# Optimization experiments

Measured on AMD Instinct MI355X. Metric: run time of the kernel, lower is better.

## Reference

```python
import jax, jax.numpy as jnp
import numpy as np

N_DIMS = 256
HW = 32
FILTERS = [32, 64, 128, 256]
SCALES = [16, 8, 4, 2]
B = 4


def _ds(t, s):
    # Exact bilinear downsample (align_corners=False, half-pixel centers) by even integer factor s:
    # target coord (i+0.5)*s - 0.5 = s*i + s/2 - 0.5 -> mean of neighbours s*i+s//2-1 and s*i+s//2.
    if s == 1:
        return t
    oH, oW = t.shape[2] // s, t.shape[3] // s
    ih = jnp.arange(oH) * s + s // 2 - 1
    iw = jnp.arange(oW) * s + s // 2 - 1
    t = 0.5 * (t[:, :, ih, :] + t[:, :, ih + 1, :])
    t = 0.5 * (t[:, :, :, iw] + t[:, :, :, iw + 1])
    return t


def _spp(t, s, w, scale, bias):
    # Upsample(1/s) -> Conv3x3(no bias) -> BN(folded to scale/bias, eval form) -> ReLU
    t = _ds(t, s)
    t = jax.lax.conv_general_dilated(t, w, (1, 1), 'SAME',
                                     dimension_numbers=('NCHW', 'OIHW', 'NCHW'))
    return jax.nn.relu(t * scale[None, :, None, None] + bias[None, :, None, None])


def setup_inputs() -> dict:
    key = jax.random.key(0)
    ks = iter(jax.random.split(key, 32))
    d = {}
    d['x'] = jax.random.normal(next(ks), (B, N_DIMS, HW, HW), jnp.float32)
    sizes = [HW * s for s in SCALES]
    for i, (c, sz) in enumerate(zip(FILTERS, sizes)):
        d[f'x{i}'] = jax.random.normal(next(ks), (B, c, sz, sz), jnp.float32)
    for i, c in enumerate(FILTERS):
        d[f'w{i}'] = jax.random.normal(next(ks), (N_DIMS, c, 3, 3), jnp.float32) * (1.0 / np.sqrt(9 * c))
        d[f's{i}'] = jax.random.normal(next(ks), (N_DIMS,), jnp.float32) * 0.1 + 1.0
        d[f'b{i}'] = jax.random.normal(next(ks), (N_DIMS,), jnp.float32) * 0.1
    dq = N_DIMS // 8
    d['qw'] = jax.random.normal(next(ks), (dq, N_DIMS), jnp.float32) * (1.0 / np.sqrt(N_DIMS))
    d['qb'] = jnp.zeros((dq,), jnp.float32)
    d['kw'] = jax.random.normal(next(ks), (dq, N_DIMS), jnp.float32) * (1.0 / np.sqrt(N_DIMS))
    d['kb'] = jnp.zeros((dq,), jnp.float32)
    d['vw'] = jax.random.normal(next(ks), (N_DIMS, N_DIMS), jnp.float32) * (1.0 / np.sqrt(N_DIMS))
    d['vb'] = jnp.zeros((N_DIMS,), jnp.float32)
    d['rel_h'] = jax.random.normal(next(ks), (1, dq, HW, 1), jnp.float32)
    d['rel_w'] = jax.random.normal(next(ks), (1, dq, 1, HW), jnp.float32)
    d['gamma'] = jax.random.normal(next(ks), (1,), jnp.float32) * 0.5  # torch inits to 0; nonzero for useful test
    return d


def reference(x, x0, x1, x2, x3,
              w0, s0, b0, w1, s1, b1, w2, s2, b2, w3, s3, b3,
              qw, qb, kw, kb, vw, vb, rel_h, rel_w, gamma):
    Bm, C, H, W = x.shape
    N = H * W
    multi_x = (_spp(x0, 16, w0, s0, b0) + _spp(x1, 8, w1, s1, b1)
               + _spp(x2, 4, w2, s2, b2) + _spp(x3, 2, w3, s3, b3))
    # 1x1 convs as channel matmuls
    q = jnp.einsum('bchw,oc->bohw', multi_x, qw) + qb[None, :, None, None]
    k = jnp.einsum('bchw,oc->bohw', x, kw) + kb[None, :, None, None]
    v = jnp.einsum('bchw,oc->bohw', x, vw) + vb[None, :, None, None]
    q = q.reshape(Bm, -1, N).transpose(0, 2, 1)          # [B, N, C/8]
    k = k.reshape(Bm, -1, N)                             # [B, C/8, N]
    v = v.reshape(Bm, C, N)                              # [B, C, N]
    energy = jnp.einsum('bnc,bcm->bnm', q, k)            # content
    pos = (rel_h + rel_w).reshape(C // 8, N)             # [C/8, N]
    energy = energy + jnp.einsum('bnc,cm->bnm', q, pos)  # + position bias
    attn = jax.nn.softmax(energy, axis=-1)               # [B, N, N]
    out = jnp.einsum('bcj,bij->bci', v, attn).reshape(Bm, C, H, W)
    out = gamma * out + x
    return out, attn
```

## Files before the change

### kernel.cpp

```cpp
#include <hip/hip_runtime.h>
#include <stdint.h>

#define BN 4
#define CC 256
#define DQ 32
#define HWD 32
#define NN 1024

typedef __attribute__((ext_vector_type(8))) short short8v;
typedef __attribute__((ext_vector_type(16))) float float16v;

#define W3OFF0 0
#define W3OFF1 73728
#define W3OFF2 221184
#define W3OFF3 516096
#define WQOFF  1105920
#define WKOFF  1114112
#define WVOFF  1122304
#define WPKTOT 1187840

#define PREP_PAD 8880
#define PREP_RPK 4640
#define PREP_XT  512
#define PREP_TOT (PREP_PAD + PREP_RPK + PREP_XT)

#define CP_CONV 512
#define CP_PROJ 144
#define CP_TOT  (CP_CONV + CP_PROJ)

#define BUFSTRIDE 10048
#define PROWS 1032

__device__ __forceinline__ short f2bf(float f) {
  union { float f; uint32_t u; } v; v.f = f;
  uint32_t r = v.u + 0x7FFFu + ((v.u >> 16) & 1u);
  return (short)(r >> 16);
}

__device__ __forceinline__ void gl_lds16(const short* g, short* l) {
  __builtin_amdgcn_global_load_lds(
      (const __attribute__((address_space(1))) void*)g,
      (__attribute__((address_space(3))) void*)l, 16, 0, 0);
}

__global__ __launch_bounds__(256) void prep_kernel(
    const float* __restrict__ x0, const float* __restrict__ x1,
    const float* __restrict__ x2, const float* __restrict__ x3,
    const float* __restrict__ w0, const float* __restrict__ w1,
    const float* __restrict__ w2, const float* __restrict__ w3,
    const float* __restrict__ qw, const float* __restrict__ kw,
    const float* __restrict__ vw, const float* __restrict__ x,
    short* __restrict__ pim, short* __restrict__ wpk,
    short* __restrict__ xT2) {
  __shared__ float t[64][33];
  int bid = blockIdx.x;
  int tid = threadIdx.x;
  if (bid < PREP_PAD) {
    int plane = bid / 37;
    int idx = (bid % 37) * 256 + tid;
    if (idx >= 9248) return;
    int b = plane / 60, g = plane % 60;
    int pr = idx / 272;
    int rem = idx % 272;
    int pc = rem >> 3, j = rem & 7;
    const float* xs;
    int s, gb, C;
    if (g < 4)       { xs = x0; s = 16; gb = 0;  C = 32; }
    else if (g < 12) { xs = x1; s = 8;  gb = 4;  C = 64; }
    else if (g < 28) { xs = x2; s = 4;  gb = 12; C = 128; }
    else             { xs = x3; s = 2;  gb = 28; C = 256; }
    float v = 0.f;
    if (pr >= 1 && pr <= 32 && pc >= 1 && pc <= 32) {
      int c = (g - gb) * 8 + j;
      int inHW = 32 * s;
      int ih = (pr - 1) * s + (s >> 1) - 1;
      int iw = (pc - 1) * s + (s >> 1) - 1;
      const float* p = xs + ((size_t)(b * C + c) * inHW + ih) * inHW + iw;
      v = 0.25f * (p[0] + p[1] + p[inHW] + p[inHW + 1]);
    }
    pim[(size_t)plane * 9248 + idx] = f2bf(v);
  } else if (bid < PREP_PAD + PREP_RPK) {
    int idx = (bid - PREP_PAD) * 256 + tid;
    if (idx >= WPKTOT) return;
    const float* w;
    int Cin, chunks, taps, ridx;
    if (idx < W3OFF1)      { w = w0; Cin = 32;  chunks = 2;  taps = 9; ridx = idx; }
    else if (idx < W3OFF2) { w = w1; Cin = 64;  chunks = 4;  taps = 9; ridx = idx - W3OFF1; }
    else if (idx < W3OFF3) { w = w2; Cin = 128; chunks = 8;  taps = 9; ridx = idx - W3OFF2; }
    else if (idx < WQOFF)  { w = w3; Cin = 256; chunks = 16; taps = 9; ridx = idx - W3OFF3; }
    else if (idx < WKOFF)  { w = qw; Cin = 256; chunks = 16; taps = 1; ridx = idx - WQOFF; }
    else if (idx < WVOFF)  { w = kw; Cin = 256; chunks = 16; taps = 1; ridx = idx - WKOFF; }
    else                   { w = vw; Cin = 256; chunks = 16; taps = 1; ridx = idx - WVOFF; }
    int per = taps * 512;
    int g2 = ridx / per;
    int rem = ridx % per;
    int tap = rem >> 9;
    int l = (rem >> 3) & 63;
    int j = rem & 7;
    int ocg = g2 / chunks;
    int chunk = g2 % chunks;
    int oc = ocg * 32 + (l & 31);
    int c = chunk * 16 + ((l >> 5) << 3) + j;
    wpk[idx] = f2bf(w[((size_t)oc * Cin + c) * taps + tap]);
  } else {
    int xb = bid - PREP_PAD - PREP_RPK;
    int nb = xb & 31;
    int cb = (xb >> 5) & 3;
    int b = xb >> 7;
    int n0 = nb * 32, c0 = cb * 64;
    int a = tid >> 5, e = tid & 31;
#pragma unroll
    for (int k = 0; k < 8; ++k)
      t[a + 8 * k][e] = x[((size_t)(b * CC + c0 + a + 8 * k) * NN) + n0 + e];
    __syncthreads();
    int n = tid & 31, cg = tid >> 5;
    short8v o;
#pragma unroll
    for (int jj = 0; jj < 8; ++jj) o[jj] = f2bf(t[cg * 8 + jj][n]);
    *(short8v*)(xT2 + (((size_t)(b * 32) + cb * 8 + cg) * 1024 + n0 + n) * 8) = o;
  }
}

template<int CHUNKS, int GB, int WOFS_>
__device__ __forceinline__ void conv_body_lds(
    const short* __restrict__ pim, const short* __restrict__ wpk,
    const float* __restrict__ sc, const float* __restrict__ bi,
    short* __restrict__ multiT4, short* lds,
    int b, int ocg, int rowq, int sp) {
  int tid = threadIdx.x;
  int w = tid >> 6, l = tid & 63;
  int col = l & 31, chH = l >> 5;
  int r0 = rowq * 8;
  int oc0 = ocg * 32;
  const short* asrc0 = wpk + WOFS_ + (size_t)(ocg * CHUNKS) * 4608;

  auto STAGE = [&](int ck, int buf) {
    short* A = lds + buf * BUFSTRIDE;
    short* B = A + 4608;
    const short* as = asrc0 + (size_t)ck * 4608;
    const short* p0 = pim + ((size_t)(b * 60 + GB + 2 * ck) * 1156 + r0 * 34) * 8;
    const short* p1 = pim + ((size_t)(b * 60 + GB + 2 * ck + 1) * 1156 + r0 * 34) * 8;
    gl_lds16(as + tid * 8, A + (size_t)w * 512);
    if (tid < 64) gl_lds16(as + (512 + tid) * 8, A + 4096);
    const short* src = (tid < 340) ? (p0 + tid * 8) : (p1 + (tid - 340) * 8);
    gl_lds16(src, B + (size_t)w * 512);
    if (tid < 168)
      gl_lds16(p1 + (172 + tid) * 8, B + 4096 + (size_t)w * 512);
  };

  float16v acc;
#pragma unroll
  for (int r = 0; r < 16; ++r) acc[r] = 0.f;

  STAGE(0, 0);
  __syncthreads();
  int cur = 0;
#pragma unroll
  for (int ck = 0; ck < CHUNKS; ++ck) {
    if (ck + 1 < CHUNKS) STAGE(ck + 1, cur ^ 1);
    const short* A = lds + cur * BUFSTRIDE;
    const short* B = A + 4608;
#pragma unroll
    for (int ky = 0; ky < 3; ++ky)
#pragma unroll
      for (int kx = 0; kx < 3; ++kx) {
        short8v av = *(const short8v*)&A[(ky * 3 + kx) * 512 + l * 8];
        short8v bv = *(const short8v*)&B[chH * 2720 + (w + ky) * 272 + (col + kx) * 8];
        acc = __builtin_amdgcn_mfma_f32_32x32x16_bf16(av, bv, acc, 0, 0, 0);
      }
    __syncthreads();
    cur ^= 1;
  }

  float* sTw = ((float*)lds) + w * (32 * 33);
#pragma unroll
  for (int r = 0; r < 16; ++r) {
    int ocl = (r & 3) + ((r >> 2) << 3) + (chH << 2);
    float t = fmaf(acc[r], sc[oc0 + ocl], bi[oc0 + ocl]);
    sTw[ocl * 33 + col] = t > 0.f ? t : 0.f;
  }
  __syncthreads();
#pragma unroll
  for (int it = 0; it < 2; ++it) {
    int idx = l + (it << 6);
    int cg = idx >> 5;
    int c2 = idx & 31;
    short8v o;
#pragma unroll
    for (int jj = 0; jj < 8; ++jj) o[jj] = f2bf(sTw[(cg * 8 + jj) * 33 + c2]);
    *(short8v*)(multiT4 + (size_t)sp * 1048576 +
                (((size_t)(b * 32) + ocg * 4 + cg) * 1024 + (r0 + w) * 32 + c2) * 8) = o;
  }
}

__global__ __launch_bounds__(512) void convproj2_kernel(
    const short* __restrict__ pim, const short* __restrict__ wpk,
    const short* __restrict__ xT2,
    const float* __restrict__ sc0, const float* __restrict__ bi0,
    const float* __restrict__ sc1, const float* __restrict__ bi1,
    const float* __restrict__ sc2, const float* __restrict__ bi2,
    const float* __restrict__ sc3, const float* __restrict__ bi3,
    const float* __restrict__ kbi, const float* __restrict__ vbi,
    const float* __restrict__ relh, const float* __restrict__ relw,
    short* __restrict__ multiT4, float* __restrict__ kpbuf,
    short* __restrict__ vbf2) {
  __shared__ short lds[2 * BUFSTRIDE];
  int bid = blockIdx.x;
  int tid = threadIdx.x;
  if (bid < CP_CONV) {
    int s = 3 - (bid >> 7);
    int cb = bid & 127;
    int rowq = cb & 3;
    int ocg = (cb >> 2) & 7;
    int b = cb >> 5;
    if (s == 3)      conv_body_lds<16, 28, W3OFF3>(pim, wpk, sc3, bi3, multiT4, lds, b, ocg, rowq, 3);
    else if (s == 2) conv_body_lds<8, 12, W3OFF2>(pim, wpk, sc2, bi2, multiT4, lds, b, ocg, rowq, 2);
    else if (s == 1) conv_body_lds<4, 4, W3OFF1>(pim, wpk, sc1, bi1, multiT4, lds, b, ocg, rowq, 1);
    else             conv_body_lds<2, 0, W3OFF0>(pim, wpk, sc0, bi0, multiT4, lds, b, ocg, rowq, 0);
  } else {
    int u = (bid - CP_CONV) * 8 + (tid >> 6);
    int l = tid & 63;
    int mode, b, nt, ocg;
    const short* ap;
    const float* bias;
    if (u < 128) { mode = 1; b = u >> 5; nt = u & 31; ocg = 0; ap = wpk + WKOFF; bias = kbi; }
    else { int t2 = u - 128; mode = 2; nt = t2 & 31; ocg = (t2 >> 5) & 7; b = t2 >> 8; ap = wpk + WVOFF + (size_t)ocg * 16 * 512; bias = vbi; }
    int n = nt * 32 + (l & 31);
    int half = l >> 5;
    ap += l * 8;
    float16v acc;
#pragma unroll
    for (int r = 0; r < 16; ++r) acc[r] = 0.f;
#pragma unroll
    for (int ck = 0; ck < 16; ++ck) {
      short8v av = *(const short8v*)(ap + ck * 512);
      short8v bv = *(const short8v*)(xT2 + (((size_t)(b * 32) + ck * 2 + half) * 1024 + n) * 8);
      acc = __builtin_amdgcn_mfma_f32_32x32x16_bf16(av, bv, acc, 0, 0, 0);
    }
#pragma unroll
    for (int r = 0; r < 16; ++r) {
      int oc = ocg * 32 + (r & 3) + ((r >> 2) << 3) + (half << 2);
      float t = acc[r] + bias[oc];
      if (mode == 1) {
        t += relh[oc * 32 + (n >> 5)] + relw[oc * 32 + (n & 31)];
        kpbuf[((size_t)b * DQ + oc) * NN + n] = t;
      } else {
        vbf2[(((size_t)(b * 128) + (n >> 3)) * 256 + oc) * 8 + (n & 7)] = f2bf(t);
      }
    }
  }
}

__global__ __launch_bounds__(256) void attnout_kernel(
    const short* __restrict__ multiT4, const short* __restrict__ wpk,
    const float* __restrict__ qbi, const float* __restrict__ kp,
    const short* __restrict__ vbf2, const float* __restrict__ x,
    const float* __restrict__ gamma, float* __restrict__ attn,
    float* __restrict__ out) {
  __shared__ union {
    float lds_q[4][32][33];
    short P[8][PROWS];
  } u;
  __shared__ float qs[DQ][8];
  __shared__ float redm[4][8], reds[4][8];
  int bidx = blockIdx.x;
  int ig = bidx & 127;
  int b = bidx >> 7;
  int i0 = ig * 8;
  int tid = threadIdx.x;
  int w = tid >> 6, l = tid & 63;
  int it0 = (ig >> 2) * 32;

  {
    int n = it0 + (l & 31);
    int half = l >> 5;
    const short* ap = wpk + WQOFF + l * 8;
    float16v acc;
#pragma unroll
    for (int r = 0; r < 16; ++r) acc[r] = 0.f;
#pragma unroll
    for (int c4 = 0; c4 < 4; ++c4) {
      int ck = w * 4 + c4;
      short8v av = *(const short8v*)(ap + ck * 512);
      size_t bix = (((size_t)(b * 32) + ck * 2 + half) * 1024 + n) * 8;
      short8v bv0 = *(const short8v*)(multiT4 + bix);
      short8v bv1 = *(const short8v*)(multiT4 + 1048576 + bix);
      short8v bv2 = *(const short8v*)(multiT4 + 2097152 + bix);
      short8v bv3 = *(const short8v*)(multiT4 + 3145728 + bix);
      acc = __builtin_amdgcn_mfma_f32_32x32x16_bf16(av, bv0, acc, 0, 0, 0);
      acc = __builtin_amdgcn_mfma_f32_32x32x16_bf16(av, bv1, acc, 0, 0, 0);
      acc = __builtin_amdgcn_mfma_f32_32x32x16_bf16(av, bv2, acc, 0, 0, 0);
      acc = __builtin_amdgcn_mfma_f32_32x32x16_bf16(av, bv3, acc, 0, 0, 0);
    }
#pragma unroll
    for (int r = 0; r < 16; ++r) {
      int oc = (r & 3) + ((r >> 2) << 3) + (half << 2);
      u.lds_q[w][oc][l & 31] = acc[r];
    }
  }
  __syncthreads();
  {
    int c = tid >> 3, rr = tid & 7;
    int nl = (ig & 3) * 8 + rr;
    qs[c][rr] = u.lds_q[0][c][nl] + u.lds_q[1][c][nl] + u.lds_q[2][c][nl] +
                u.lds_q[3][c][nl] + qbi[c];
  }
  __syncthreads();

  float e[8][4];
#pragma unroll
  for (int r = 0; r < 8; ++r)
#pragma unroll
    for (int k = 0; k < 4; ++k) e[r][k] = 0.f;
  const float* kpb = kp + (size_t)b * DQ * NN + tid;
  for (int c = 0; c < DQ; ++c) {
    float k0 = kpb[0], k1 = kpb[256], k2 = kpb[512], k3 = kpb[768];
    kpb += NN;
#pragma unroll
    for (int r = 0; r < 8; ++r) {
      float qv = qs[c][r];
      e[r][0] = fmaf(qv, k0, e[r][0]);
      e[r][1] = fmaf(qv, k1, e[r][1]);
      e[r][2] = fmaf(qv, k2, e[r][2]);
      e[r][3] = fmaf(qv, k3, e[r][3]);
    }
  }
  int lane = tid & 63, wvi = tid >> 6;
#pragma unroll
  for (int r = 0; r < 8; ++r) {
    float mm = fmaxf(fmaxf(e[r][0], e[r][1]), fmaxf(e[r][2], e[r][3]));
#pragma unroll
    for (int off = 32; off > 0; off >>= 1) mm = fmaxf(mm, __shfl_xor(mm, off));
    if (lane == 0) redm[wvi][r] = mm;
  }
  __syncthreads();
#pragma unroll
  for (int r = 0; r < 8; ++r) {
    float mm = fmaxf(fmaxf(redm[0][r], redm[1][r]), fmaxf(redm[2][r], redm[3][r]));
    float ss = 0.f;
#pragma unroll
    for (int k = 0; k < 4; ++k) {
      e[r][k] = __expf(e[r][k] - mm);
      ss += e[r][k];
    }
#pragma unroll
    for (int off = 32; off > 0; off >>= 1) ss += __shfl_xor(ss, off);
    if (lane == 0) reds[wvi][r] = ss;
  }
  __syncthreads();
#pragma unroll
  for (int r = 0; r < 8; ++r) {
    float inv = 1.f / (reds[0][r] + reds[1][r] + reds[2][r] + reds[3][r]);
    int i = i0 + r;
    size_t base = ((size_t)b * NN + i) * NN + tid;
#pragma unroll
    for (int k = 0; k < 4; ++k) {
      float av = e[r][k] * inv;
      attn[base + k * 256] = av;
      u.P[r][tid + k * 256] = f2bf(av);
    }
  }
  __syncthreads();

  {
    int half = l >> 5, lane31 = l & 31;
    float g = gamma[0];
    const short* prow = &u.P[lane31 & 7][half * 8];
#pragma unroll
    for (int ct = 0; ct < 2; ++ct) {
      int c0 = (w * 2 + ct) * 32;
      const short* vbase = vbf2 + (((size_t)(b * 128) + half) * 256 + c0 + lane31) * 8;
      float16v acc;
#pragma unroll
      for (int r = 0; r < 16; ++r) acc[r] = 0.f;
#pragma unroll 4
      for (int jc = 0; jc < 64; ++jc) {
        short8v av = *(const short8v*)(vbase + (size_t)jc * 2 * 256 * 8);
        short8v bv = *(const short8v*)(prow + jc * 16);
        acc = __builtin_amdgcn_mfma_f32_32x32x16_bf16(av, bv, acc, 0, 0, 0);
      }
      if (lane31 < 8) {
        int i = i0 + lane31;
#pragma unroll
        for (int r = 0; r < 16; ++r) {
          int c = c0 + (r & 3) + ((r >> 2) << 3) + (half << 2);
          size_t off = ((size_t)b * CC + c) * NN + i;
          out[off] = fmaf(g, acc[r], x[off]);
        }
      }
    }
  }
}

extern "C" void kernel_launch(void* const* d_in, const int* in_sizes, int n_in,
                              void* d_out, int out_size, void* d_ws, size_t ws_size,
                              hipStream_t stream) {
  const float* x    = (const float*)d_in[0];
  const float* x0   = (const float*)d_in[1];
  const float* x1   = (const float*)d_in[2];
  const float* x2   = (const float*)d_in[3];
  const float* x3   = (const float*)d_in[4];
  const float* w0   = (const float*)d_in[5];
  const float* s0   = (const float*)d_in[6];
  const float* b0   = (const float*)d_in[7];
  const float* w1   = (const float*)d_in[8];
  const float* s1   = (const float*)d_in[9];
  const float* b1   = (const float*)d_in[10];
  const float* w2   = (const float*)d_in[11];
  const float* s2   = (const float*)d_in[12];
  const float* b2   = (const float*)d_in[13];
  const float* w3   = (const float*)d_in[14];
  const float* s3   = (const float*)d_in[15];
  const float* b3   = (const float*)d_in[16];
  const float* qw   = (const float*)d_in[17];
  const float* qbi  = (const float*)d_in[18];
  const float* kw   = (const float*)d_in[19];
  const float* kbi  = (const float*)d_in[20];
  const float* vw   = (const float*)d_in[21];
  const float* vbi  = (const float*)d_in[22];
  const float* relh = (const float*)d_in[23];
  const float* relw = (const float*)d_in[24];
  const float* gamma= (const float*)d_in[25];

  float* ws = (float*)d_ws;
  short* pim     = (short*)ws;
  short* multiT4 = (short*)(ws + 1109760);
  float* kpbuf   = ws + 3337984;
  short* xT2     = (short*)(ws + 3469056);
  short* vbf2    = (short*)(ws + 3993344);
  short* wpk     = (short*)(ws + 4517632);

  float* out  = (float*)d_out;
  float* attn = out + (size_t)BN * CC * NN;

  prep_kernel<<<PREP_TOT, 256, 0, stream>>>(x0, x1, x2, x3, w0, w1, w2, w3,
                                            qw, kw, vw, x, pim, wpk, xT2);

  convproj2_kernel<<<CP_TOT, 512, 0, stream>>>(pim, wpk, xT2,
                                               s0, b0, s1, b1, s2, b2, s3, b3,
                                               kbi, vbi, relh, relw,
                                               multiT4, kpbuf, vbf2);

  attnout_kernel<<<512, 256, 0, stream>>>(multiT4, wpk, qbi, kpbuf,
                                          vbf2, x, gamma, attn, out);
}
```

Baseline: 82.79 us.

## Process 16 query rows per block with 512 threads in attention kernel

The attention/output kernel now handles 16 query rows per block using 8 waves instead of 8 rows with 4 waves, halving the block count to 256. Each K element loaded is reused across 16 rows, and each wave computes one 32-channel tile of the PV product instead of two, so V loads are amortised over twice as many rows. The Q projection still uses only 4 waves, so half the block idles during that phase. The grid of 256 blocks may underfill a GPU with many compute units.

```diff
diff --git a/kernel.cpp b/kernel.cpp
--- a/kernel.cpp
+++ b/kernel.cpp
@@ -251,7 +251,7 @@
   }
 }
 
-__global__ __launch_bounds__(256) void attnout_kernel(
+__global__ __launch_bounds__(512) void attnout2_kernel(
     const short* __restrict__ multiT4, const short* __restrict__ wpk,
     const float* __restrict__ qbi, const float* __restrict__ kp,
     const short* __restrict__ vbf2, const float* __restrict__ x,
@@ -259,19 +259,19 @@
     float* __restrict__ out) {
   __shared__ union {
     float lds_q[4][32][33];
-    short P[8][PROWS];
+    short P[16][PROWS];
   } u;
-  __shared__ float qs[DQ][8];
-  __shared__ float redm[4][8], reds[4][8];
+  __shared__ float qs[DQ][16];
+  __shared__ float redm[8][16], reds[8][16];
   int bidx = blockIdx.x;
-  int ig = bidx & 127;
-  int b = bidx >> 7;
-  int i0 = ig * 8;
+  int ig = bidx & 63;
+  int b = bidx >> 6;
+  int i0 = ig * 16;
   int tid = threadIdx.x;
   int w = tid >> 6, l = tid & 63;
-  int it0 = (ig >> 2) * 32;
-
-  {
+  int it0 = (ig >> 1) * 32;
+
+  if (w < 4) {
     int n = it0 + (l & 31);
     int half = l >> 5;
     const short* ap = wpk + WQOFF + l * 8;
@@ -300,93 +300,86 @@
   }
   __syncthreads();
   {
-    int c = tid >> 3, rr = tid & 7;
-    int nl = (ig & 3) * 8 + rr;
+    int c = tid >> 4, rr = tid & 15;
+    int nl = (ig & 1) * 16 + rr;
     qs[c][rr] = u.lds_q[0][c][nl] + u.lds_q[1][c][nl] + u.lds_q[2][c][nl] +
                 u.lds_q[3][c][nl] + qbi[c];
   }
   __syncthreads();
 
-  float e[8][4];
-#pragma unroll
-  for (int r = 0; r < 8; ++r)
-#pragma unroll
-    for (int k = 0; k < 4; ++k) e[r][k] = 0.f;
+  float e[16][2];
+#pragma unroll
+  for (int r = 0; r < 16; ++r) { e[r][0] = 0.f; e[r][1] = 0.f; }
   const float* kpb = kp + (size_t)b * DQ * NN + tid;
   for (int c = 0; c < DQ; ++c) {
-    float k0 = kpb[0], k1 = kpb[256], k2 = kpb[512], k3 = kpb[768];
+    float k0 = kpb[0], k1 = kpb[512];
     kpb += NN;
 #pragma unroll
-    for (int r = 0; r < 8; ++r) {
+    for (int r = 0; r < 16; ++r) {
       float qv = qs[c][r];
       e[r][0] = fmaf(qv, k0, e[r][0]);
       e[r][1] = fmaf(qv, k1, e[r][1]);
-      e[r][2] = fmaf(qv, k2, e[r][2]);
-      e[r][3] = fmaf(qv, k3, e[r][3]);
-    }
-  }
-  int lane = tid & 63, wvi = tid >> 6;
-#pragma unroll
-  for (int r = 0; r < 8; ++r) {
-    float mm = fmaxf(fmaxf(e[r][0], e[r][1]), fmaxf(e[r][2], e[r][3]));
+    }
+  }
+#pragma unroll
+  for (int r = 0; r < 16; ++r) {
+    float mm = fmaxf(e[r][0], e[r][1]);
 #pragma unroll
     for (int off = 32; off > 0; off >>= 1) mm = fmaxf(mm, __shfl_xor(mm, off));
-    if (lane == 0) redm[wvi][r] = mm;
-  }
-  __syncthreads();
-#pragma unroll
-  for (int r = 0; r < 8; ++r) {
-    float mm = fmaxf(fmaxf(redm[0][r], redm[1][r]), fmaxf(redm[2][r], redm[3][r]));
-    float ss = 0.f;
-#pragma unroll
-    for (int k = 0; k < 4; ++k) {
-      e[r][k] = __expf(e[r][k] - mm);
-      ss += e[r][k];
-    }
+    if (l == 0) redm[w][r] = mm;
+  }
+  __syncthreads();
+#pragma unroll
+  for (int r = 0; r < 16; ++r) {
+    float mm = redm[0][r];
+#pragma unroll
+    for (int q = 1; q < 8; ++q) mm = fmaxf(mm, redm[q][r]);
+    e[r][0] = __expf(e[r][0] - mm);
+    e[r][1] = __expf(e[r][1] - mm);
+    float ss = e[r][0] + e[r][1];
 #pragma unroll
     for (int off = 32; off > 0; off >>= 1) ss += __shfl_xor(ss, off);
-    if (lane == 0) reds[wvi][r] = ss;
-  }
-  __syncthreads();
-#pragma unroll
-  for (int r = 0; r < 8; ++r) {
-    float inv = 1.f / (reds[0][r] + reds[1][r] + reds[2][r] + reds[3][r]);
+    if (l == 0) reds[w][r] = ss;
+  }
+  __syncthreads();
+#pragma unroll
+  for (int r = 0; r < 16; ++r) {
+    float ss = reds[0][r];
+#pragma unroll
+    for (int q = 1; q < 8; ++q) ss += reds[q][r];
+    float inv = 1.f / ss;
     int i = i0 + r;
     size_t base = ((size_t)b * NN + i) * NN + tid;
-#pragma unroll
-    for (int k = 0; k < 4; ++k) {
-      float av = e[r][k] * inv;
-      attn[base + k * 256] = av;
-      u.P[r][tid + k * 256] = f2bf(av);
-    }
+    float a0 = e[r][0] * inv, a1 = e[r][1] * inv;
+    attn[base] = a0;
+    attn[base + 512] = a1;
+    u.P[r][tid] = f2bf(a0);
+    u.P[r][tid + 512] = f2bf(a1);
   }
   __syncthreads();
 
   {
     int half = l >> 5, lane31 = l & 31;
     float g = gamma[0];
-    const short* prow = &u.P[lane31 & 7][half * 8];
-#pragma unroll
-    for (int ct = 0; ct < 2; ++ct) {
-      int c0 = (w * 2 + ct) * 32;
-      const short* vbase = vbf2 + (((size_t)(b * 128) + half) * 256 + c0 + lane31) * 8;
-      float16v acc;
-#pragma unroll
-      for (int r = 0; r < 16; ++r) acc[r] = 0.f;
+    int c0 = w * 32;
+    const short* vbase = vbf2 + (((size_t)(b * 128) + half) * 256 + c0 + lane31) * 8;
+    const short* prow = &u.P[lane31 & 15][half * 8];
+    float16v acc;
+#pragma unroll
+    for (int r = 0; r < 16; ++r) acc[r] = 0.f;
 #pragma unroll 4
-      for (int jc = 0; jc < 64; ++jc) {
-        short8v av = *(const short8v*)(vbase + (size_t)jc * 2 * 256 * 8);
-        short8v bv = *(const short8v*)(prow + jc * 16);
-        acc = __builtin_amdgcn_mfma_f32_32x32x16_bf16(av, bv, acc, 0, 0, 0);
-      }
-      if (lane31 < 8) {
-        int i = i0 + lane31;
-#pragma unroll
-        for (int r = 0; r < 16; ++r) {
-          int c = c0 + (r & 3) + ((r >> 2) << 3) + (half << 2);
-          size_t off = ((size_t)b * CC + c) * NN + i;
-          out[off] = fmaf(g, acc[r], x[off]);
-        }
+    for (int jc = 0; jc < 64; ++jc) {
+      short8v av = *(const short8v*)(vbase + (size_t)jc * 2 * 256 * 8);
+      short8v bv = *(const short8v*)(prow + jc * 16);
+      acc = __builtin_amdgcn_mfma_f32_32x32x16_bf16(av, bv, acc, 0, 0, 0);
+    }
+    if (lane31 < 16) {
+      int i = i0 + lane31;
+#pragma unroll
+      for (int r = 0; r < 16; ++r) {
+        int c = c0 + (r & 3) + ((r >> 2) << 3) + (half << 2);
+        size_t off = ((size_t)b * CC + c) * NN + i;
+        out[off] = fmaf(g, acc[r], x[off]);
       }
     }
   }
@@ -441,6 +434,6 @@
                                                kbi, vbi, relh, relw,
                                                multiT4, kpbuf, vbf2);
 
-  attnout_kernel<<<512, 256, 0, stream>>>(multiT4, wpk, qbi, kpbuf,
-                                          vbf2, x, gamma, attn, out);
-}
+  attnout2_kernel<<<256, 512, 0, stream>>>(multiT4, wpk, qbi, kpbuf,
+                                           vbf2, x, gamma, attn, out);
+}
```

Result: faster. 74.47 us, median of 2 (-10.0%).
